# Kernel tuning notes

Measured on AMD Instinct MI355X. Metric: run time of the kernel, lower is better.

The kernel has to match this reference:

```python
import jax, jax.numpy as jnp
import numpy as np
from jax import lax

HEADS = 8

# Haar-lifting 4x4 matrices from nlwt_init / inlwt_init
U1P1 = jnp.array([[-0.5, -0.5, -0.5, 0.5], [0.5, -0.5, 0.5, 0.5], [0.5, 0.5, -0.5, 0.5], [0.5, -0.5, -0.5, -0.5]], jnp.float32)
U2P2 = jnp.array([[-1., 1., 1., -1.], [-1., -1., -1., -1.], [-1., -1., 1., 1.], [1., -1., 1., -1.]], jnp.float32)
P2U2 = jnp.array([[-1., -1., -1., 1.], [1., -1., -1., -1.], [1., -1., 1., 1.], [-1., -1., 1., -1.]], jnp.float32)
P1U1 = jnp.array([[-0.125, 0.125, 0.125, 0.125], [-0.125, -0.125, 0.125, -0.125], [-0.125, 0.125, -0.125, -0.125], [0.125, 0.125, 0.125, -0.125]], jnp.float32)


def conv1x1(x, w):
    # w: [out_ch, in_ch]
    return jnp.einsum('oi,bihw->bohw', w, x)


def dwconv3(x, w):
    # depthwise 3x3, w: [C,1,3,3]
    return lax.conv_general_dilated(x, w, (1, 1), [(1, 1), (1, 1)],
                                    dimension_numbers=('NCHW', 'OIHW', 'NCHW'),
                                    feature_group_count=x.shape[1])


def layernorm_c(x, w, b):
    # WithBias LayerNorm over channel dim (to_3d normalizes last dim == c)
    mu = jnp.mean(x, axis=1, keepdims=True)
    var = jnp.var(x, axis=1, keepdims=True)
    return (x - mu) / jnp.sqrt(var + 1e-5) * w[None, :, None, None] + b[None, :, None, None]


def attention(x, temperature, qkv_w, qkv_dw_w, proj_w):
    b, c, h, w = x.shape
    qkv = dwconv3(conv1x1(x, qkv_w), qkv_dw_w)
    q, k, v = jnp.split(qkv, 3, axis=1)
    hd = lambda t: t.reshape(b, HEADS, c // HEADS, h * w)
    q, k, v = hd(q), hd(k), hd(v)
    q = q / jnp.maximum(jnp.linalg.norm(q, axis=-1, keepdims=True), 1e-12)
    k = k / jnp.maximum(jnp.linalg.norm(k, axis=-1, keepdims=True), 1e-12)
    attn = jax.nn.softmax(jnp.einsum('bhcn,bhdn->bhcd', q, k) * temperature, axis=-1)
    out = jnp.einsum('bhcd,bhdn->bhcn', attn, v).reshape(b, c, h, w)
    return conv1x1(out, proj_w)


def ffn(x, pin_w, dw_w, pout_w):
    y = dwconv3(conv1x1(x, pin_w), dw_w)
    y1, y2 = jnp.split(y, 2, axis=1)
    return conv1x1(jax.nn.gelu(y1, approximate=False) * y2, pout_w)


def tblock(x, ln1_w, ln1_b, temperature, qkv_w, qkv_dw_w, proj_w, ln2_w, ln2_b, pin_w, ffn_dw_w, pout_w):
    x = x + attention(layernorm_c(x, ln1_w, ln1_b), temperature, qkv_w, qkv_dw_w, proj_w)
    x = x + ffn(layernorm_c(x, ln2_w, ln2_b), pin_w, ffn_dw_w, pout_w)
    return x


def nlwt(x):
    # lifting wavelet decompose (nlwt_init), vectorized im2col via reshape
    b, c, h, w = x.shape
    h1, w1 = h // 2, w // 2
    col = x.reshape(b, c, h1, 2, w1, 2).transpose(0, 1, 3, 5, 2, 4).reshape(b, c, 4, h1 * w1)
    x1 = jnp.einsum('ij,bcjn->bcin', U1P1, col).reshape(b, c, 4, h1, w1)
    t1 = x1[:, :, 0]
    t2 = jnp.roll(x1[:, :, 1], -1, axis=2)
    t3 = jnp.roll(x1[:, :, 2], -1, axis=3)
    t4 = jnp.roll(x1[:, :, 3], (-1, -1), axis=(2, 3))
    x1 = jnp.stack([t1, t2, t3, t4], axis=2).reshape(b, c, 4, h1 * w1)
    x2 = jnp.einsum('ij,bcjn->bcin', U2P2, x1).reshape(b, c, 4, h1, w1)
    return x2[:, :, 0], x2[:, :, 1], x2[:, :, 2], x2[:, :, 3]


def inlwt(A, B, C, D):
    # lifting wavelet reconstruct (inlwt_init), vectorized col2im via reshape
    b, c, h1, w1 = A.shape
    Y1 = jnp.stack([A, B, C, D], axis=2).reshape(b, c, 4, h1 * w1)
    Y2 = jnp.einsum('ij,bcjn->bcin', P2U2, Y1).reshape(b, c, 4, h1, w1)
    t1 = Y2[:, :, 0]
    t2 = jnp.roll(Y2[:, :, 1], 1, axis=2)
    t3 = jnp.roll(Y2[:, :, 2], 1, axis=3)
    t4 = jnp.roll(Y2[:, :, 3], (1, 1), axis=(2, 3))
    Y2 = jnp.stack([t1, t2, t3, t4], axis=2).reshape(b, c, 4, h1 * w1)
    Y3 = jnp.einsum('ij,bcjn->bcin', P1U1, Y2).reshape(b, c, 2, 2, h1, w1)
    return Y3.transpose(0, 1, 4, 2, 5, 3).reshape(b, c, 2 * h1, 2 * w1)


def gfm(x1, x2, ca_w1, ca_w2, sa_w, sa_b):
    Cc = x1.shape[1]
    cat = jnp.concatenate([x1, x2], axis=1)  # [b, 2C, h, w]
    avg = jnp.mean(cat, axis=(2, 3), keepdims=True)
    mx = jnp.max(cat, axis=(2, 3), keepdims=True)
    mlp = lambda t: conv1x1(jax.nn.relu(conv1x1(t, ca_w1)), ca_w2)
    cw = jax.nn.sigmoid(mlp(avg) + mlp(mx))  # [b, 2C, 1, 1]
    cw = cw.reshape(-1, 2, Cc)[:, :, :, None, None]
    out = cw[:, 0] * x1 + cw[:, 1] * x2
    savg = jnp.mean(out, axis=1, keepdims=True)
    smax = jnp.max(out, axis=1, keepdims=True)
    sa = lax.conv_general_dilated(jnp.concatenate([savg, smax], axis=1), sa_w, (1, 1), [(3, 3), (3, 3)],
                                  dimension_numbers=('NCHW', 'OIHW', 'NCHW')) + sa_b[None, :, None, None]
    return jax.nn.sigmoid(sa) * out


def setup_inputs() -> dict:
    key = jax.random.key(0)
    ks = jax.random.split(key, 16)
    B, C, H, W = 2, 48, 256, 256
    hidden = int(C * 2.66)  # 127
    s = 0.05
    return {
        'x': jax.random.normal(ks[0], (B, C, H, W), jnp.float32),
        'ln1_w': jnp.ones((C,), jnp.float32),
        'ln1_b': jnp.zeros((C,), jnp.float32),
        'temperature': jnp.ones((HEADS, 1, 1), jnp.float32),
        'qkv_w': jax.random.normal(ks[1], (3 * C, C), jnp.float32) * s,
        'qkv_dw_w': jax.random.normal(ks[2], (3 * C, 1, 3, 3), jnp.float32) * s,
        'proj_w': jax.random.normal(ks[3], (C, C), jnp.float32) * s,
        'ln2_w': jnp.ones((C,), jnp.float32),
        'ln2_b': jnp.zeros((C,), jnp.float32),
        'pin_w': jax.random.normal(ks[4], (2 * hidden, C), jnp.float32) * s,
        'ffn_dw_w': jax.random.normal(ks[5], (2 * hidden, 1, 3, 3), jnp.float32) * s,
        'pout_w': jax.random.normal(ks[6], (C, hidden), jnp.float32) * s,
        'ca_w1': jax.random.normal(ks[7], (2 * C // 16, 2 * C), jnp.float32) * s,
        'ca_w2': jax.random.normal(ks[8], (2 * C, 2 * C // 16), jnp.float32) * s,
        'sa_w': jax.random.normal(ks[9], (1, 2, 7, 7), jnp.float32) * s,
        'sa_b': jnp.zeros((1,), jnp.float32),
    }


def reference(x, ln1_w, ln1_b, temperature, qkv_w, qkv_dw_w, proj_w, ln2_w, ln2_b, pin_w, ffn_dw_w, pout_w, ca_w1, ca_w2, sa_w, sa_b):
    tb = lambda t: tblock(t, ln1_w, ln1_b, temperature, qkv_w, qkv_dw_w, proj_w, ln2_w, ln2_b, pin_w, ffn_dw_w, pout_w)
    branch1 = tb(x)
    A, Bh, Ch, Dh = nlwt(x)
    branch2 = inlwt(tb(A), Bh, Ch, Dh)
    return gfm(branch1, branch2, ca_w1, ca_w2, sa_w, sa_b)
```

## Files before the change

### kernel.cpp

```cpp
#include <hip/hip_runtime.h>
#include <math.h>

namespace {

constexpr int BB   = 2;
constexpr int CC   = 48;
constexpr int NHEAD= 8;
constexpr int CPH  = 6;
constexpr int HID  = 127;
constexpr int QKVC = 144;
constexpr int PINC = 254;
constexpr int N1   = 256*256;
constexpr int N2   = 128*128;
constexpr size_t PS2 = (size_t)BB*CC*N2;
constexpr size_t NB1 = (size_t)BB*CC*N1;

__device__ __forceinline__ float b2f(unsigned short u) {
    unsigned int x = ((unsigned int)u) << 16;
    float f; __builtin_memcpy(&f, &x, 4); return f;
}
__device__ __forceinline__ unsigned short f2b(float f) {
    unsigned int x; __builtin_memcpy(&x, &f, 4);
    unsigned int r = (x + 0x7FFFu + ((x >> 16) & 1u)) >> 16;
    return (unsigned short)r;
}
__device__ __forceinline__ unsigned int pack2(float lo, float hi) {
    return (unsigned int)f2b(lo) | ((unsigned int)f2b(hi) << 16);
}

__device__ __forceinline__ float gelu_t(float x) {
    float z = 1.5957691216057308f * (x + 0.044715f * x * x * x);
    float e = __expf(z);
    return x * (1.0f - 1.0f / (e + 1.0f));
}

__global__ void k_zero(float* __restrict__ p, int n)
{
    int i = blockIdx.x*256 + threadIdx.x;
    if (i < n) p[i] = 0.f;
}

__global__ void k_repw(const float* __restrict__ w, float* __restrict__ wt, int O, int K)
{
    int i = blockIdx.x*256 + threadIdx.x;
    if (i < O*K) {
        int c = i / O, oc = i - c*O;
        wt[c*O + oc] = w[oc*K + c];
    }
}

__global__ __launch_bounds__(256) void k_ln(const float* __restrict__ X,
                       const float* __restrict__ lw, const float* __restrict__ lb,
                       unsigned short* __restrict__ xh, int Ns)
{
    int g = blockIdx.x*256 + threadIdx.x;
    int half = Ns >> 1;
    int b = g / half, pp = (g - b*half)*2;
    const float* xb = X + (size_t)b*CC*Ns + pp;
    float v0[CC], v1[CC];
    float s0=0.f, s20=0.f, s1=0.f, s21=0.f;
#pragma unroll
    for (int c = 0; c < CC; ++c) {
        float2 v = *(const float2*)(xb + (size_t)c*Ns);
        v0[c]=v.x; v1[c]=v.y;
        s0 += v.x; s20 = fmaf(v.x,v.x,s20);
        s1 += v.y; s21 = fmaf(v.y,v.y,s21);
    }
    float mu0 = s0*(1.0f/CC), mu1 = s1*(1.0f/CC);
    float i0 = 1.0f/sqrtf(s20*(1.0f/CC)-mu0*mu0+1e-5f);
    float i1 = 1.0f/sqrtf(s21*(1.0f/CC)-mu1*mu1+1e-5f);
    unsigned short* ob = xh + (size_t)b*CC*Ns + pp;
#pragma unroll
    for (int c = 0; c < CC; ++c) {
        float w = lw[c], bb2 = lb[c];
        float y0 = (v0[c]-mu0)*i0*w + bb2;
        float y1 = (v1[c]-mu1)*i1*w + bb2;
        *(unsigned int*)(ob + (size_t)c*Ns) = pack2(y0, y1);
    }
}

template<int OC, int CH>
__device__ __forceinline__ void conv2_acc(const unsigned short* __restrict__ xb, int Ns,
                                          const float* __restrict__ wt, int ocb,
                                          unsigned short* __restrict__ ob)
{
    float a0[CH], a1[CH];
#pragma unroll
    for (int i = 0; i < CH; ++i) { a0[i]=0.f; a1[i]=0.f; }
#pragma unroll
    for (int c0 = 0; c0 < CC; c0 += 8) {
        unsigned int gv[8];
#pragma unroll
        for (int u = 0; u < 8; ++u)
            gv[u] = *(const unsigned int*)(xb + (size_t)(c0+u)*Ns);
#pragma unroll
        for (int u = 0; u < 8; ++u) {
            float t0 = b2f((unsigned short)(gv[u] & 0xffffu));
            float t1 = b2f((unsigned short)(gv[u] >> 16));
            const float* wr = wt + (c0+u)*OC + ocb;
#pragma unroll
            for (int i = 0; i < CH; ++i) {
                float w = wr[i];
                a0[i] = fmaf(t0, w, a0[i]);
                a1[i] = fmaf(t1, w, a1[i]);
            }
        }
    }
#pragma unroll
    for (int i = 0; i < CH; ++i)
        *(unsigned int*)(ob + (size_t)(ocb+i)*Ns) = pack2(a0[i], a1[i]);
}

template<int OC>
__global__ __launch_bounds__(256) void k_conv1x1(const unsigned short* __restrict__ xh,
                       const float* __restrict__ wt, unsigned short* __restrict__ out, int Ns)
{
    int g = blockIdx.x*256 + threadIdx.x;
    int half = Ns >> 1;
    int b = g / half, pp = (g - b*half)*2;
    int ocb = blockIdx.y * 16;
    const unsigned short* xb = xh + (size_t)b*CC*Ns + pp;
    unsigned short* ob = out + (size_t)b*OC*Ns + pp;
    constexpr int R = (OC % 16 == 0) ? 16 : (OC % 16);
    if (ocb + 16 <= OC) conv2_acc<OC,16>(xb, Ns, wt, ocb, ob);
    else                conv2_acc<OC,R >(xb, Ns, wt, ocb, ob);
}

__device__ __forceinline__ void load_row10(const unsigned short* __restrict__ p,
                                           bool rok, bool lok, bool rrok, float (&f)[10])
{
    if (rok) {
        uint4 cv = *(const uint4*)p;
        unsigned int u0=cv.x,u1=cv.y,u2=cv.z,u3=cv.w;
        f[1]=b2f((unsigned short)(u0&0xffffu)); f[2]=b2f((unsigned short)(u0>>16));
        f[3]=b2f((unsigned short)(u1&0xffffu)); f[4]=b2f((unsigned short)(u1>>16));
        f[5]=b2f((unsigned short)(u2&0xffffu)); f[6]=b2f((unsigned short)(u2>>16));
        f[7]=b2f((unsigned short)(u3&0xffffu)); f[8]=b2f((unsigned short)(u3>>16));
        f[0] = lok  ? b2f(p[-1]) : 0.f;
        f[9] = rrok ? b2f(p[8])  : 0.f;
    } else {
#pragma unroll
        for (int i = 0; i < 10; ++i) f[i] = 0.f;
    }
}

__device__ __forceinline__ void dw8(const unsigned short* __restrict__ plane,
                                    const float* __restrict__ w9,
                                    int y, int x0, int Hs, int Ws, float (&o)[8])
{
#pragma unroll
    for (int i = 0; i < 8; ++i) o[i] = 0.f;
#pragma unroll
    for (int dy = 0; dy < 3; ++dy) {
        int r = y + dy - 1;
        bool rok = (r >= 0) && (r < Hs);
        float f[10];
        const unsigned short* p = plane + (size_t)(rok ? r : 0)*Ws + x0;
        load_row10(p, rok, x0 > 0, x0 + 8 < Ws, f);
        float w0 = w9[dy*3], w1 = w9[dy*3+1], w2 = w9[dy*3+2];
#pragma unroll
        for (int i = 0; i < 8; ++i)
            o[i] = fmaf(f[i], w0, fmaf(f[i+1], w1, fmaf(f[i+2], w2, o[i])));
    }
}

__global__ __launch_bounds__(256) void k_dw3v(const unsigned short* __restrict__ in,
                      const float* __restrict__ w,
                      float* __restrict__ out, int nch, int Hs, int Ws)
{
    int Ns = Hs * Ws, ng = Ns >> 3, wq = Ws >> 3;
    int g = blockIdx.x*256 + threadIdx.x;
    int t = g % ng, bc = g / ng;
    int c = bc % nch;
    int y = t / wq, x0 = (t - y*wq) << 3;
    float o[8];
    dw8(in + (size_t)bc*Ns, w + c*9, y, x0, Hs, Ws, o);
    float4* ob = (float4*)(out + (size_t)bc*Ns + y*Ws + x0);
    ob[0] = make_float4(o[0],o[1],o[2],o[3]);
    ob[1] = make_float4(o[4],o[5],o[6],o[7]);
}

__global__ __launch_bounds__(256) void k_dwgate(const unsigned short* __restrict__ pin,
                         const float* __restrict__ dww,
                         unsigned short* __restrict__ gate, int Hs, int Ws)
{
    int Ns = Hs * Ws, ng = Ns >> 3, wq = Ws >> 3;
    int g = blockIdx.x*256 + threadIdx.x;
    int t = g % ng, bc = g / ng;
    int b = bc / HID, c = bc - b*HID;
    int y = t / wq, x0 = (t - y*wq) << 3;
    float d1[8], d2[8];
    dw8(pin + ((size_t)b*PINC + c)*Ns,       dww + c*9,         y, x0, Hs, Ws, d1);
    dw8(pin + ((size_t)b*PINC + HID + c)*Ns, dww + (c+HID)*9,   y, x0, Hs, Ws, d2);
    uint4 r;
    r.x = pack2(gelu_t(d1[0])*d2[0], gelu_t(d1[1])*d2[1]);
    r.y = pack2(gelu_t(d1[2])*d2[2], gelu_t(d1[3])*d2[3]);
    r.z = pack2(gelu_t(d1[4])*d2[4], gelu_t(d1[5])*d2[5]);
    r.w = pack2(gelu_t(d1[6])*d2[6], gelu_t(d1[7])*d2[7]);
    *(uint4*)(gate + (size_t)bc*Ns + y*Ws + x0) = r;
}

__global__ __launch_bounds__(256) void k_qk_stats(const float* __restrict__ qkvd,
                                                  float* __restrict__ st, int Ns)
{
    const int NBLK = 32;
    int bh = blockIdx.x / NBLK, blk = blockIdx.x % NBLK;
    int b = bh / NHEAD, h = bh % NHEAD;
    const float* qb = qkvd + ((size_t)b*QKVC + h*CPH)*Ns;
    const float* kb = qkvd + ((size_t)b*QKVC + 48 + h*CPH)*Ns;
    float vals[48];
#pragma unroll
    for (int i = 0; i < 48; ++i) vals[i] = 0.f;
    for (int n = blk*256 + (int)threadIdx.x; n < Ns; n += NBLK*256) {
        float qv[CPH], kv[CPH];
#pragma unroll
        for (int i = 0; i < CPH; ++i) { qv[i] = qb[(size_t)i*Ns + n]; kv[i] = kb[(size_t)i*Ns + n]; }
#pragma unroll
        for (int i = 0; i < CPH; ++i) {
            vals[i]   = fmaf(qv[i], qv[i], vals[i]);
            vals[6+i] = fmaf(kv[i], kv[i], vals[6+i]);
        }
#pragma unroll
        for (int i = 0; i < CPH; ++i)
#pragma unroll
            for (int j = 0; j < CPH; ++j)
                vals[12 + i*6 + j] = fmaf(qv[i], kv[j], vals[12 + i*6 + j]);
    }
    __shared__ float red[4][48];
    int lane = threadIdx.x & 63, wave = threadIdx.x >> 6;
#pragma unroll
    for (int i = 0; i < 48; ++i) {
        float v = vals[i];
#pragma unroll
        for (int off = 32; off > 0; off >>= 1) v += __shfl_down(v, off);
        if (lane == 0) red[wave][i] = v;
    }
    __syncthreads();
    if ((int)threadIdx.x < 48) {
        int i = threadIdx.x;
        float v = red[0][i] + red[1][i] + red[2][i] + red[3][i];
        float* dst;
        if (i < 6)       dst = st + b*48 + h*CPH + i;
        else if (i < 12) dst = st + 96 + b*48 + h*CPH + (i-6);
        else             dst = st + 192 + (b*NHEAD+h)*36 + (i-12);
        atomicAdd(dst, v);
    }
}

__global__ void k_attn(const float* __restrict__ st, const float* __restrict__ temp,
                       float* __restrict__ ao)
{
    int t = threadIdx.x;
    if (t >= BB*NHEAD) return;
    int b = t / NHEAD, h = t % NHEAD;
    const float* sqq = st + b*48 + h*CPH;
    const float* sqk = st + 96 + b*48 + h*CPH;
    const float* g   = st + 192 + (b*NHEAD+h)*36;
    float T = temp[h];
    float nq[CPH], nk[CPH];
#pragma unroll
    for (int i = 0; i < CPH; ++i) {
        nq[i] = fmaxf(sqrtf(sqq[i]), 1e-12f);
        nk[i] = fmaxf(sqrtf(sqk[i]), 1e-12f);
    }
    float* out = ao + (b*NHEAD+h)*36;
#pragma unroll
    for (int c = 0; c < CPH; ++c) {
        float l[CPH]; float m = -1e30f;
#pragma unroll
        for (int d = 0; d < CPH; ++d) {
            l[d] = g[c*6+d] / (nq[c]*nk[d]) * T;
            m = fmaxf(m, l[d]);
        }
        float ssum = 0.f;
#pragma unroll
        for (int d = 0; d < CPH; ++d) { l[d] = expf(l[d]-m); ssum += l[d]; }
        float r = 1.0f/ssum;
#pragma unroll
        for (int d = 0; d < CPH; ++d) out[c*6+d] = l[d]*r;
    }
}

__global__ __launch_bounds__(256) void k_av_proj(const float* __restrict__ qkvd, const float* __restrict__ attn,
                          const float* __restrict__ projw, const float* __restrict__ X,
                          float* __restrict__ x1, int Ns)
{
    int g = blockIdx.x*256 + threadIdx.x;
    int b = g / Ns, p = g - b*Ns;
    int ocb = blockIdx.y * 16;
    const float* vb = qkvd + ((size_t)b*QKVC + 96)*Ns + p;
    float vv[CC];
#pragma unroll
    for (int c = 0; c < CC; ++c) vv[c] = vb[(size_t)c*Ns];
    const float* at = attn + b*288;
    float o[CC];
#pragma unroll
    for (int h = 0; h < NHEAD; ++h)
#pragma unroll
        for (int cc = 0; cc < CPH; ++cc) {
            float acc = 0.f;
#pragma unroll
            for (int d = 0; d < CPH; ++d)
                acc = fmaf(at[(h*CPH+cc)*CPH + d], vv[h*CPH + d], acc);
            o[h*CPH+cc] = acc;
        }
    const float* xb = X + (size_t)b*CC*Ns + p;
    float* ob = x1 + (size_t)b*CC*Ns + p;
    float acc[16];
#pragma unroll
    for (int i = 0; i < 16; ++i) acc[i] = 0.f;
#pragma unroll
    for (int c = 0; c < CC; ++c) {
#pragma unroll
        for (int i = 0; i < 16; ++i)
            acc[i] = fmaf(o[c], projw[(ocb+i)*CC + c], acc[i]);
    }
#pragma unroll
    for (int i = 0; i < 16; ++i)
        ob[(size_t)(ocb+i)*Ns] = xb[(size_t)(ocb+i)*Ns] + acc[i];
}

template<int U>
__device__ __forceinline__ void pout_chunk(const unsigned short* __restrict__ gb, int c0, int Ns,
                                           const float* __restrict__ wt, int ocb,
                                           float (&a0)[16], float (&a1)[16])
{
    unsigned int gv[U];
#pragma unroll
    for (int u = 0; u < U; ++u)
        gv[u] = *(const unsigned int*)(gb + (size_t)(c0+u)*Ns);
#pragma unroll
    for (int u = 0; u < U; ++u) {
        float t0 = b2f((unsigned short)(gv[u] & 0xffffu));
        float t1 = b2f((unsigned short)(gv[u] >> 16));
        const float* wr = wt + (c0+u)*48 + ocb;
#pragma unroll
        for (int i = 0; i < 16; ++i) {
            float w = wr[i];
            a0[i] = fmaf(t0, w, a0[i]);
            a1[i] = fmaf(t1, w, a1[i]);
        }
    }
}

__global__ __launch_bounds__(256) void k_pout(const unsigned short* __restrict__ gate,
                       const float* __restrict__ wt, const float* __restrict__ x1,
                       float* __restrict__ out, int Ns)
{
    int g = blockIdx.x*256 + threadIdx.x;
    int half = Ns >> 1;
    int b = g / half, pp = (g - b*half)*2;
    int ocb = blockIdx.y * 16;
    const unsigned short* gb = gate + (size_t)b*HID*Ns + pp;
    float a0[16], a1[16];
#pragma unroll
    for (int i = 0; i < 16; ++i) { a0[i] = 0.f; a1[i] = 0.f; }
    int c = 0;
    for (; c + 8 <= HID; c += 8)
        pout_chunk<8>(gb, c, Ns, wt, ocb, a0, a1);
    pout_chunk<7>(gb, c, Ns, wt, ocb, a0, a1);
    const float* xb = x1 + (size_t)b*CC*Ns + pp;
    float* ob = out + (size_t)b*CC*Ns + pp;
#pragma unroll
    for (int i = 0; i < 16; ++i) {
        float2 xv = *(const float2*)(xb + (size_t)(ocb+i)*Ns);
        float2 o; o.x = xv.x + a0[i]; o.y = xv.y + a1[i];
        *(float2*)(ob + (size_t)(ocb+i)*Ns) = o;
    }
}

__global__ __launch_bounds__(256) void k_nlwt(const float* __restrict__ X, float* __restrict__ A4)
{
    int g = blockIdx.x*256 + threadIdx.x;
    int n = g & (N2-1); int bc = g >> 14;
    int h1 = n >> 7, w1 = n & 127;
    int hb = (h1+1)&127, wb = (w1+1)&127;
    const float* xp = X + (size_t)bc * N1;
    float t1, t2, t3, t4;
    {
        int y=h1, z=w1;
        float c0=xp[(2*y)*256+2*z], c1=xp[(2*y)*256+2*z+1], c2=xp[(2*y+1)*256+2*z], c3=xp[(2*y+1)*256+2*z+1];
        t1 = 0.5f*(-c0 - c1 - c2 + c3);
    }
    {
        int y=hb, z=w1;
        float c0=xp[(2*y)*256+2*z], c1=xp[(2*y)*256+2*z+1], c2=xp[(2*y+1)*256+2*z], c3=xp[(2*y+1)*256+2*z+1];
        t2 = 0.5f*( c0 - c1 + c2 + c3);
    }
    {
        int y=h1, z=wb;
        float c0=xp[(2*y)*256+2*z], c1=xp[(2*y)*256+2*z+1], c2=xp[(2*y+1)*256+2*z], c3=xp[(2*y+1)*256+2*z+1];
        t3 = 0.5f*( c0 + c1 - c2 + c3);
    }
    {
        int y=hb, z=wb;
        float c0=xp[(2*y)*256+2*z], c1=xp[(2*y)*256+2*z+1], c2=xp[(2*y+1)*256+2*z], c3=xp[(2*y+1)*256+2*z+1];
        t4 = 0.5f*( c0 - c1 - c2 - c3);
    }
    size_t o = (size_t)bc*N2 + n;
    A4[o]           = -t1 + t2 + t3 - t4;
    A4[PS2 + o]     = -t1 - t2 - t3 - t4;
    A4[2*PS2 + o]   = -t1 - t2 + t3 + t4;
    A4[3*PS2 + o]   =  t1 - t2 + t3 - t4;
}

__global__ __launch_bounds__(256) void k_inlwt(const float* __restrict__ Ain, const float* __restrict__ A4,
                        float* __restrict__ out)
{
    int g = blockIdx.x*256 + threadIdx.x;
    int n = g & (N2-1); int bc = g >> 14;
    int h1 = n >> 7, w1 = n & 127;
    int hm = (h1-1)&127, wm = (w1-1)&127;
    const float* I0 = Ain + (size_t)bc*N2;
    const float* I1 = A4 + PS2   + (size_t)bc*N2;
    const float* I2 = A4 + 2*PS2 + (size_t)bc*N2;
    const float* I3 = A4 + 3*PS2 + (size_t)bc*N2;
    int i00 = h1*128+w1, i10 = hm*128+w1, i01 = h1*128+wm, i11 = hm*128+wm;
    float t1, t2, t3, t4;
    { float a=I0[i00], b2=I1[i00], c2=I2[i00], d2=I3[i00]; t1 = -a - b2 - c2 + d2; }
    { float a=I0[i10], b2=I1[i10], c2=I2[i10], d2=I3[i10]; t2 =  a - b2 - c2 - d2; }
    { float a=I0[i01], b2=I1[i01], c2=I2[i01], d2=I3[i01]; t3 =  a - b2 + c2 + d2; }
    { float a=I0[i11], b2=I1[i11], c2=I2[i11], d2=I3[i11]; t4 = -a - b2 + c2 - d2; }
    float y00 = 0.125f*(-t1 + t2 + t3 + t4);
    float y01 = 0.125f*(-t1 - t2 + t3 - t4);
    float y10 = 0.125f*(-t1 + t2 - t3 - t4);
    float y11 = 0.125f*( t1 + t2 + t3 - t4);
    float* ob = out + (size_t)bc * N1;
    int oy = h1*2, ox = w1*2;
    ob[(size_t)oy*256 + ox]       = y00;
    ob[(size_t)oy*256 + ox + 1]   = y01;
    ob[(size_t)(oy+1)*256 + ox]   = y10;
    ob[(size_t)(oy+1)*256 + ox+1] = y11;
}

constexpr int CSEG = 8;
__global__ __launch_bounds__(256) void k_chstat_part(const float* __restrict__ b1, const float* __restrict__ b2,
                         float* __restrict__ ps, float* __restrict__ pm)
{
    int bc = blockIdx.x;
    int seg = blockIdx.y;
    int b = bc / 96, ch = bc % 96;
    const float* src = (ch < 48 ? b1 + ((size_t)b*CC + ch)*N1
                                : b2 + ((size_t)b*CC + (ch-48))*N1) + (size_t)seg*(N1/CSEG);
    const float4* s4 = (const float4*)src;
    float s = 0.f, m = -1e30f;
    for (int i = threadIdx.x; i < N1/CSEG/4; i += 256) {
        float4 v = s4[i];
        s += v.x+v.y+v.z+v.w;
        m = fmaxf(m, fmaxf(fmaxf(v.x,v.y), fmaxf(v.z,v.w)));
    }
    int lane = threadIdx.x & 63, wave = threadIdx.x >> 6;
    __shared__ float rs[4], rm[4];
#pragma unroll
    for (int off = 32; off > 0; off >>= 1) {
        s += __shfl_down(s, off);
        m = fmaxf(m, __shfl_down(m, off));
    }
    if (lane == 0) { rs[wave] = s; rm[wave] = m; }
    __syncthreads();
    if (threadIdx.x == 0) {
        ps[bc*CSEG + seg] = rs[0]+rs[1]+rs[2]+rs[3];
        pm[bc*CSEG + seg] = fmaxf(fmaxf(rm[0],rm[1]), fmaxf(rm[2],rm[3]));
    }
}

__global__ void k_chstat_fin(const float* __restrict__ ps, const float* __restrict__ pm,
                             float* __restrict__ avg, float* __restrict__ mxo)
{
    int t = threadIdx.x;
    if (t >= BB*96) return;
    float s = 0.f, m = -1e30f;
#pragma unroll
    for (int j = 0; j < CSEG; ++j) {
        s += ps[t*CSEG+j];
        m = fmaxf(m, pm[t*CSEG+j]);
    }
    avg[t] = s*(1.0f/N1);
    mxo[t] = m;
}

__global__ void k_cw(const float* __restrict__ avg, const float* __restrict__ mx,
                     const float* __restrict__ w1, const float* __restrict__ w2,
                     float* __restrict__ cw)
{
    int t = threadIdx.x;
    if (t >= BB*96) return;
    int b = t / 96, o = t % 96;
    float ta[6], tm[6];
#pragma unroll
    for (int j = 0; j < 6; ++j) {
        float sa = 0.f, sm = 0.f;
        for (int i = 0; i < 96; ++i) {
            float w = w1[j*96+i];
            sa = fmaf(w, avg[b*96+i], sa);
            sm = fmaf(w, mx[b*96+i], sm);
        }
        ta[j] = sa > 0.f ? sa : 0.f;
        tm[j] = sm > 0.f ? sm : 0.f;
    }
    float ua = 0.f, um = 0.f;
#pragma unroll
    for (int j = 0; j < 6; ++j) {
        ua = fmaf(w2[o*6+j], ta[j], ua);
        um = fmaf(w2[o*6+j], tm[j], um);
    }
    float z = ua + um;
    cw[t] = 1.0f/(1.0f+expf(-z));
}

__global__ __launch_bounds__(256) void k_gfm_out(const float* __restrict__ b1, const float* __restrict__ b2,
                          const float* __restrict__ cw, float* __restrict__ ob,
                          float* __restrict__ savg, float* __restrict__ smax)
{
    int g = blockIdx.x*256 + threadIdx.x;
    int b = g >> 16, p = g & (N1-1);
    float s = 0.f, m = -1e30f;
#pragma unroll
    for (int c = 0; c < CC; ++c) {
        size_t idx = ((size_t)b*CC + c)*N1 + p;
        float o = cw[b*96 + c]*b1[idx] + cw[b*96 + 48 + c]*b2[idx];
        ob[idx] = o;
        s += o; m = fmaxf(m, o);
    }
    savg[(size_t)b*N1 + p] = s*(1.0f/CC);
    smax[(size_t)b*N1 + p] = m;
}

__global__ __launch_bounds__(256) void k_final(const float* __restrict__ savg, const float* __restrict__ smax,
                        const float* __restrict__ saw, const float* __restrict__ sab,
                        const float* __restrict__ ob, float* __restrict__ out)
{
    int g = blockIdx.x*256 + threadIdx.x;
    int b = g >> 16, p = g & (N1-1);
    int y = p >> 8, x = p & 255;
    float s = sab[0];
    const float* av = savg + (size_t)b*N1;
    const float* mx = smax + (size_t)b*N1;
#pragma unroll
    for (int ky = 0; ky < 7; ++ky) {
        int yy = y + ky - 3;
        bool yok = (yy >= 0) && (yy < 256);
        int yc = yy < 0 ? 0 : (yy > 255 ? 255 : yy);
#pragma unroll
        for (int kx = 0; kx < 7; ++kx) {
            int xx = x + kx - 3;
            bool ok = yok && (xx >= 0) && (xx < 256);
            int xc = xx < 0 ? 0 : (xx > 255 ? 255 : xx);
            int idx = yc*256 + xc;
            float a = av[idx], m2 = mx[idx];
            s = fmaf(ok ? a  : 0.f, saw[ky*7+kx], s);
            s = fmaf(ok ? m2 : 0.f, saw[49 + ky*7+kx], s);
        }
    }
    float sig = 1.0f/(1.0f+expf(-s));
#pragma unroll
    for (int c = 0; c < CC; ++c) {
        size_t idx = ((size_t)b*CC + c)*N1 + p;
        out[idx] = sig * ob[idx];
    }
}

}

extern "C" void kernel_launch(void* const* d_in, const int* in_sizes, int n_in,
                              void* d_out, int out_size, void* d_ws, size_t ws_size,
                              hipStream_t stream)
{
    const float* x    = (const float*)d_in[0];
    const float* ln1w = (const float*)d_in[1];
    const float* ln1b = (const float*)d_in[2];
    const float* temp = (const float*)d_in[3];
    const float* qkvw = (const float*)d_in[4];
    const float* qkvdw= (const float*)d_in[5];
    const float* projw= (const float*)d_in[6];
    const float* ln2w = (const float*)d_in[7];
    const float* ln2b = (const float*)d_in[8];
    const float* pinw = (const float*)d_in[9];
    const float* ffdw = (const float*)d_in[10];
    const float* poutw= (const float*)d_in[11];
    const float* caw1 = (const float*)d_in[12];
    const float* caw2 = (const float*)d_in[13];
    const float* saw  = (const float*)d_in[14];
    const float* sab  = (const float*)d_in[15];

    float* wsf  = (float*)d_ws;
    float* A4   = wsf;
    float* br1  = A4 + 4*PS2;
    float* br2  = br1 + NB1;
    float* x1b  = br2 + NB1;
    float* tbA  = x1b + NB1;
    float* qkv  = tbA + PS2;
    float* qkvd = qkv + (size_t)BB*QKVC*N1;
    float* stats= qkvd + (size_t)BB*QKVC*N1;
    float* wqr  = stats + 4096;
    float* wpr  = wqr + 48*QKVC;
    float* wor  = wpr + 48*PINC;
    float* chps = wor + HID*48;
    float* chpm = chps + 192*CSEG;
    float* savg = chpm + 192*CSEG;
    float* smax = savg + (size_t)BB*N1;

    k_repw<<<(48*QKVC+255)/256, 256, 0, stream>>>(qkvw, wqr, QKVC, 48);
    k_repw<<<(48*PINC+255)/256, 256, 0, stream>>>(pinw, wpr, PINC, 48);
    k_repw<<<(HID*48+255)/256, 256, 0, stream>>>(poutw, wor, 48, HID);

    auto tb = [&](const float* Xin, float* outp, int Hs, int Ws) {
        int Ns = Hs*Ws;
        int npix = BB*Ns;
        unsigned short* xhat = (unsigned short*)qkvd;
        k_zero<<<3, 256, 0, stream>>>(stats, 768);
        k_ln<<<npix/512, 256, 0, stream>>>(Xin, ln1w, ln1b, xhat, Ns);
        dim3 gq(npix/512, QKVC/16);
        k_conv1x1<QKVC><<<gq, 256, 0, stream>>>(xhat, wqr, (unsigned short*)qkv, Ns);
        k_dw3v<<<(BB*QKVC*Ns/8)/256, 256, 0, stream>>>((const unsigned short*)qkv, qkvdw, qkvd, QKVC, Hs, Ws);
        k_qk_stats<<<BB*NHEAD*32, 256, 0, stream>>>(qkvd, stats, Ns);
        k_attn<<<1, 64, 0, stream>>>(stats, temp, stats + 768);
        dim3 g4(npix/256, 3);
        k_av_proj<<<g4, 256, 0, stream>>>(qkvd, stats + 768, projw, Xin, x1b, Ns);
        k_ln<<<npix/512, 256, 0, stream>>>(x1b, ln2w, ln2b, xhat, Ns);
        dim3 gp(npix/512, (PINC+15)/16);
        k_conv1x1<PINC><<<gp, 256, 0, stream>>>(xhat, wpr, (unsigned short*)qkv, Ns);
        k_dwgate<<<(BB*HID*Ns/8)/256, 256, 0, stream>>>((const unsigned short*)qkv, ffdw,
                                                        (unsigned short*)qkvd, Hs, Ws);
        dim3 g6(npix/512, 3);
        k_pout<<<g6, 256, 0, stream>>>((const unsigned short*)qkvd, wor, x1b, outp, Ns);
    };

    tb(x, br1, 256, 256);
    k_nlwt<<<(BB*CC*N2)/256, 256, 0, stream>>>(x, A4);
    tb(A4, tbA, 128, 128);
    k_inlwt<<<(BB*CC*N2)/256, 256, 0, stream>>>(tbA, A4, br2);
    dim3 gc(BB*96, CSEG);
    k_chstat_part<<<gc, 256, 0, stream>>>(br1, br2, chps, chpm);
    k_chstat_fin<<<1, 256, 0, stream>>>(chps, chpm, stats + 1344, stats + 1536);
    k_cw<<<1, 256, 0, stream>>>(stats + 1344, stats + 1536, caw1, caw2, stats + 1728);
    k_gfm_out<<<(BB*N1)/256, 256, 0, stream>>>(br1, br2, stats + 1728, x1b, savg, smax);
    k_final<<<(BB*N1)/256, 256, 0, stream>>>(savg, smax, saw, sab, x1b, (float*)d_out);
}
```

Baseline: 498.3 us.

## Use bf16 MFMA for 1x1 convs with pixel-major layernorm output

Result: faster. 430.2 us (-13.7%).

```diff
diff --git a/kernel.cpp b/kernel.cpp
--- a/kernel.cpp
+++ b/kernel.cpp
@@ -15,6 +15,9 @@
 constexpr size_t PS2 = (size_t)BB*CC*N2;
 constexpr size_t NB1 = (size_t)BB*CC*N1;
 
+using short8  = __attribute__((ext_vector_type(8))) short;
+using floatx4 = __attribute__((ext_vector_type(4))) float;
+
 __device__ __forceinline__ float b2f(unsigned short u) {
     unsigned int x = ((unsigned int)u) << 16;
     float f; __builtin_memcpy(&f, &x, 4); return f;
@@ -49,7 +52,28 @@
     }
 }
 
-__global__ __launch_bounds__(256) void k_ln(const float* __restrict__ X,
+template<int OCR, int OCT>
+__global__ void k_packw_mfma(const float* __restrict__ w, unsigned short* __restrict__ wf)
+{
+    int i = blockIdx.x*256 + threadIdx.x;
+    if (i >= OCT*2*64) return;
+    int lane = i & 63, ts = i >> 6;
+    int s = ts & 1, t = ts >> 1;
+    int oc = t*16 + (lane & 15);
+    int kb = s*32 + (lane >> 4)*8;
+    float v[8];
+#pragma unroll
+    for (int j = 0; j < 8; ++j) {
+        int k = kb + j;
+        v[j] = (oc < OCR && k < 48) ? w[oc*48 + k] : 0.f;
+    }
+    uint4 o;
+    o.x = pack2(v[0], v[1]); o.y = pack2(v[2], v[3]);
+    o.z = pack2(v[4], v[5]); o.w = pack2(v[6], v[7]);
+    *(uint4*)(wf + (size_t)i*8) = o;
+}
+
+__global__ __launch_bounds__(256) void k_ln_t(const float* __restrict__ X,
                        const float* __restrict__ lw, const float* __restrict__ lb,
                        unsigned short* __restrict__ xh, int Ns)
 {
@@ -69,61 +93,58 @@
     float mu0 = s0*(1.0f/CC), mu1 = s1*(1.0f/CC);
     float i0 = 1.0f/sqrtf(s20*(1.0f/CC)-mu0*mu0+1e-5f);
     float i1 = 1.0f/sqrtf(s21*(1.0f/CC)-mu1*mu1+1e-5f);
-    unsigned short* ob = xh + (size_t)b*CC*Ns + pp;
-#pragma unroll
-    for (int c = 0; c < CC; ++c) {
-        float w = lw[c], bb2 = lb[c];
-        float y0 = (v0[c]-mu0)*i0*w + bb2;
-        float y1 = (v1[c]-mu1)*i1*w + bb2;
-        *(unsigned int*)(ob + (size_t)c*Ns) = pack2(y0, y1);
-    }
-}
-
-template<int OC, int CH>
-__device__ __forceinline__ void conv2_acc(const unsigned short* __restrict__ xb, int Ns,
-                                          const float* __restrict__ wt, int ocb,
-                                          unsigned short* __restrict__ ob)
-{
-    float a0[CH], a1[CH];
-#pragma unroll
-    for (int i = 0; i < CH; ++i) { a0[i]=0.f; a1[i]=0.f; }
-#pragma unroll
-    for (int c0 = 0; c0 < CC; c0 += 8) {
-        unsigned int gv[8];
-#pragma unroll
-        for (int u = 0; u < 8; ++u)
-            gv[u] = *(const unsigned int*)(xb + (size_t)(c0+u)*Ns);
-#pragma unroll
-        for (int u = 0; u < 8; ++u) {
-            float t0 = b2f((unsigned short)(gv[u] & 0xffffu));
-            float t1 = b2f((unsigned short)(gv[u] >> 16));
-            const float* wr = wt + (c0+u)*OC + ocb;
-#pragma unroll
-            for (int i = 0; i < CH; ++i) {
-                float w = wr[i];
-                a0[i] = fmaf(t0, w, a0[i]);
-                a1[i] = fmaf(t1, w, a1[i]);
-            }
-        }
-    }
-#pragma unroll
-    for (int i = 0; i < CH; ++i)
-        *(unsigned int*)(ob + (size_t)(ocb+i)*Ns) = pack2(a0[i], a1[i]);
-}
-
-template<int OC>
-__global__ __launch_bounds__(256) void k_conv1x1(const unsigned short* __restrict__ xh,
-                       const float* __restrict__ wt, unsigned short* __restrict__ out, int Ns)
-{
-    int g = blockIdx.x*256 + threadIdx.x;
-    int half = Ns >> 1;
-    int b = g / half, pp = (g - b*half)*2;
-    int ocb = blockIdx.y * 16;
-    const unsigned short* xb = xh + (size_t)b*CC*Ns + pp;
-    unsigned short* ob = out + (size_t)b*OC*Ns + pp;
-    constexpr int R = (OC % 16 == 0) ? 16 : (OC % 16);
-    if (ocb + 16 <= OC) conv2_acc<OC,16>(xb, Ns, wt, ocb, ob);
-    else                conv2_acc<OC,R >(xb, Ns, wt, ocb, ob);
+    unsigned short* r0 = xh + ((size_t)b*Ns + pp)*48;
+    unsigned short* r1 = r0 + 48;
+#pragma unroll
+    for (int j = 0; j < 6; ++j) {
+        uint4 o0, o1;
+        float y[8], z[8];
+#pragma unroll
+        for (int e = 0; e < 8; ++e) {
+            int c = j*8 + e;
+            float w = lw[c], bb2 = lb[c];
+            y[e] = (v0[c]-mu0)*i0*w + bb2;
+            z[e] = (v1[c]-mu1)*i1*w + bb2;
+        }
+        o0.x = pack2(y[0],y[1]); o0.y = pack2(y[2],y[3]);
+        o0.z = pack2(y[4],y[5]); o0.w = pack2(y[6],y[7]);
+        o1.x = pack2(z[0],z[1]); o1.y = pack2(z[2],z[3]);
+        o1.z = pack2(z[4],z[5]); o1.w = pack2(z[6],z[7]);
+        *(uint4*)(r0 + j*8) = o0;
+        *(uint4*)(r1 + j*8) = o1;
+    }
+}
+
+template<int OCR, int OCT>
+__global__ __launch_bounds__(256) void k_conv_mfma(const unsigned short* __restrict__ xh,
+                       const unsigned short* __restrict__ wf,
+                       unsigned short* __restrict__ out, int Ns)
+{
+    int wid = (blockIdx.x*256 + (int)threadIdx.x) >> 6;
+    int lane = threadIdx.x & 63;
+    int tpb = Ns >> 4;
+    int b = wid / tpb, pxt = wid - b*tpb;
+    int px0 = pxt << 4;
+    int col = lane & 15, grp = lane >> 4;
+    const unsigned short* xb = xh + ((size_t)b*Ns + px0 + col)*48 + grp*8;
+    short8 b0 = *(const short8*)(xb);
+    short8 b1 = *(const short8*)(xb + 32);
+    unsigned short* ob = out + (size_t)b*OCR*Ns + px0 + col;
+    int ocb0 = grp*4;
+#pragma unroll
+    for (int t = 0; t < OCT; ++t) {
+        floatx4 acc = {};
+        short8 a0 = *(const short8*)(wf + (size_t)((t*2+0)*64 + lane)*8);
+        short8 a1 = *(const short8*)(wf + (size_t)((t*2+1)*64 + lane)*8);
+        acc = __builtin_amdgcn_mfma_f32_16x16x32_bf16(a0, b0, acc, 0, 0, 0);
+        acc = __builtin_amdgcn_mfma_f32_16x16x32_bf16(a1, b1, acc, 0, 0, 0);
+#pragma unroll
+        for (int r = 0; r < 4; ++r) {
+            int oc = t*16 + ocb0 + r;
+            if (OCR % 16 == 0 || oc < OCR)
+                ob[(size_t)oc*Ns] = f2b(acc[r]);
+        }
+    }
 }
 
 __device__ __forceinline__ void load_row10(const unsigned short* __restrict__ p,
@@ -592,16 +613,19 @@
     float* qkv  = tbA + PS2;
     float* qkvd = qkv + (size_t)BB*QKVC*N1;
     float* stats= qkvd + (size_t)BB*QKVC*N1;
-    float* wqr  = stats + 4096;
-    float* wpr  = wqr + 48*QKVC;
-    float* wor  = wpr + 48*PINC;
+    float* wfqf = stats + 4096;
+    float* wfpf = wfqf + 4608;
+    float* wor  = wfpf + 8192;
     float* chps = wor + HID*48;
     float* chpm = chps + 192*CSEG;
     float* savg = chpm + 192*CSEG;
     float* smax = savg + (size_t)BB*N1;
 
-    k_repw<<<(48*QKVC+255)/256, 256, 0, stream>>>(qkvw, wqr, QKVC, 48);
-    k_repw<<<(48*PINC+255)/256, 256, 0, stream>>>(pinw, wpr, PINC, 48);
+    unsigned short* wfq = (unsigned short*)wfqf;
+    unsigned short* wfp = (unsigned short*)wfpf;
+
+    k_packw_mfma<QKVC, 9><<<(9*2*64+255)/256, 256, 0, stream>>>(qkvw, wfq);
+    k_packw_mfma<PINC, 16><<<(16*2*64+255)/256, 256, 0, stream>>>(pinw, wfp);
     k_repw<<<(HID*48+255)/256, 256, 0, stream>>>(poutw, wor, 48, HID);
 
     auto tb = [&](const float* Xin, float* outp, int Hs, int Ws) {
@@ -609,17 +633,15 @@
         int npix = BB*Ns;
         unsigned short* xhat = (unsigned short*)qkvd;
         k_zero<<<3, 256, 0, stream>>>(stats, 768);
-        k_ln<<<npix/512, 256, 0, stream>>>(Xin, ln1w, ln1b, xhat, Ns);
-        dim3 gq(npix/512, QKVC/16);
-        k_conv1x1<QKVC><<<gq, 256, 0, stream>>>(xhat, wqr, (unsigned short*)qkv, Ns);
+        k_ln_t<<<npix/512, 256, 0, stream>>>(Xin, ln1w, ln1b, xhat, Ns);
+        k_conv_mfma<QKVC, 9><<<npix/64, 256, 0, stream>>>(xhat, wfq, (unsigned short*)qkv, Ns);
         k_dw3v<<<(BB*QKVC*Ns/8)/256, 256, 0, stream>>>((const unsigned short*)qkv, qkvdw, qkvd, QKVC, Hs, Ws);
         k_qk_stats<<<BB*NHEAD*32, 256, 0, stream>>>(qkvd, stats, Ns);
         k_attn<<<1, 64, 0, stream>>>(stats, temp, stats + 768);
         dim3 g4(npix/256, 3);
         k_av_proj<<<g4, 256, 0, stream>>>(qkvd, stats + 768, projw, Xin, x1b, Ns);
-        k_ln<<<npix/512, 256, 0, stream>>>(x1b, ln2w, ln2b, xhat, Ns);
-        dim3 gp(npix/512, (PINC+15)/16);
-        k_conv1x1<PINC><<<gp, 256, 0, stream>>>(xhat, wpr, (unsigned short*)qkv, Ns);
+        k_ln_t<<<npix/512, 256, 0, stream>>>(x1b, ln2w, ln2b, xhat, Ns);
+        k_conv_mfma<PINC, 16><<<npix/64, 256, 0, stream>>>(xhat, wfp, (unsigned short*)qkv, Ns);
         k_dwgate<<<(BB*HID*Ns/8)/256, 256, 0, stream>>>((const unsigned short*)qkv, ffdw,
                                                         (unsigned short*)qkvd, Hs, Ws);
         dim3 g6(npix/512, 3);
```
